# Optimization experiments

Measured on AMD Instinct MI355X. Metric: run time of the kernel, lower is better.

## Reference

```python
import jax, jax.numpy as jnp
import numpy as np

NU, NI, NR = 50000, 50000, 5   # users, items, rating levels
D, B, LS, LI = 64, 512, 32, 64 # embed_dim, batch, max social nbrs, max item hist
NEG = -1e9


def setup_inputs() -> dict:
    key = jax.random.key(0)
    ks = iter(jax.random.split(key, 64))
    def lin(din, dout):
        s = 1.0 / np.sqrt(din)
        return (jax.random.uniform(next(ks), (din, dout), minval=-s, maxval=s, dtype=jnp.float32),
                jax.random.uniform(next(ks), (dout,), minval=-s, maxval=s, dtype=jnp.float32))
    inp = {}
    inp['user_w'] = jax.random.normal(next(ks), (NU, D), dtype=jnp.float32) * 0.1
    inp['item_w'] = jax.random.normal(next(ks), (NI, D), dtype=jnp.float32) * 0.1
    inp['rating_w'] = jax.random.normal(next(ks), (NR, D), dtype=jnp.float32) * 0.1
    for name, din, dout in [('i_ln1', 2*D, D), ('i_ln2', D, D), ('i_ln3', 2*D, D),
                            ('i_att1', 2*D, D), ('i_att2', D, D), ('i_att3', D, 1),
                            ('s_ln1', D, D), ('s_ln2', 2*D, D), ('s_ln3', D, D),
                            ('s_att1', 2*D, D), ('s_att2', D, D), ('s_att3', D, 1)]:
        w, b = lin(din, dout)
        inp[name + '_w'] = w
        inp[name + '_b'] = b
    inp['nodes'] = jax.random.randint(next(ks), (B,), 0, NU)
    inp['social_hist'] = jax.random.randint(next(ks), (NU, LS), 0, NU)
    inp['social_mask'] = jax.random.bernoulli(next(ks), 0.5, (NU, LS)).at[:, 0].set(True)
    inp['item_hist'] = jax.random.randint(next(ks), (NU, LI), 0, NI)
    inp['rating_hist'] = jax.random.randint(next(ks), (NU, LI), 0, NR)
    inp['item_mask'] = jax.random.bernoulli(next(ks), 0.5, (NU, LI)).at[:, 0].set(True)
    return inp


def reference(user_w, item_w, rating_w,
              i_ln1_w, i_ln1_b, i_ln2_w, i_ln2_b, i_ln3_w, i_ln3_b,
              i_att1_w, i_att1_b, i_att2_w, i_att2_b, i_att3_w, i_att3_b,
              s_ln1_w, s_ln1_b, s_ln2_w, s_ln2_b, s_ln3_w, s_ln3_b,
              s_att1_w, s_att1_b, s_att2_w, s_att2_b, s_att3_w, s_att3_b,
              nodes, social_hist, social_mask, item_hist, rating_hist, item_mask):
    relu = jax.nn.relu

    def attn(x, w1, b1, w2, b2, w3, b3, mask):
        # x: [..., L, 2D] -> softmax weights over valid neighbors: [..., L]
        h = relu(x @ w1 + b1)
        h = relu(h @ w2 + b2)
        logit = (h @ w3 + b3)[..., 0]
        logit = jnp.where(mask, logit, NEG)
        return jax.nn.softmax(logit, axis=-1)

    def item_final(uids):
        # uids: any shape [...]; returns [..., D]  (Aggre_item.item_final)
        its, rts, m = item_hist[uids], rating_hist[uids], item_mask[uids]
        x = jnp.concatenate([item_w[its], rating_w[rts]], axis=-1)   # [...,LI,2D]
        x = relu(x @ i_ln1_w + i_ln1_b)                              # [...,LI,D]
        u = user_w[uids]                                             # [...,D]
        a_in = jnp.concatenate([x, jnp.broadcast_to(u[..., None, :], x.shape)], axis=-1)
        alpha = attn(a_in, i_att1_w, i_att1_b, i_att2_w, i_att2_b, i_att3_w, i_att3_b, m)
        hI = jnp.einsum('...l,...ld->...d', alpha, x)                # attention-weighted sum
        hI = relu(hI @ i_ln2_w + i_ln2_b)
        return relu(jnp.concatenate([u, hI], axis=-1) @ i_ln3_w + i_ln3_b)

    # item-space factor of query users
    hI_self = item_final(nodes)                                      # [B,D]
    # social aggregation: item_final over each user's social neighbors
    nbrs, nmask = social_hist[nodes], social_mask[nodes]             # [B,LS]
    hI_nb = item_final(nbrs)                                         # [B,LS,D]
    u = user_w[nodes]                                                # [B,D]
    b_in = jnp.concatenate([hI_nb, jnp.broadcast_to(u[:, None, :], hI_nb.shape)], axis=-1)
    beta = attn(b_in, s_att1_w, s_att1_b, s_att2_w, s_att2_b, s_att3_w, s_att3_b, nmask)
    hS = jnp.einsum('bl,bld->bd', beta, hI_nb)
    hS = relu(hS @ s_ln1_w + s_ln1_b)
    f = jnp.concatenate([hI_self, hS], axis=-1)
    f = relu(f @ s_ln2_w + s_ln2_b)
    return relu(f @ s_ln3_w + s_ln3_b)
```

## Files before the change

kernel.cpp:

```cpp
#include <hip/hip_runtime.h>
#include <math.h>


#define NII 50000
#define BB 512
#define LSS 32
#define NT 16896

typedef short short8 __attribute__((ext_vector_type(8)));
typedef float f32x4 __attribute__((ext_vector_type(4)));

static __device__ __forceinline__ bool mread(const void* p, long i, int mode) {
  if (mode == 0) return ((const int*)p)[i] != 0;
  if (mode == 2) return ((const float*)p)[i] != 0.0f;
  return ((const unsigned char*)p)[i] != 0;
}

static __device__ __forceinline__ float wsum(float v) {
#pragma unroll
  for (int s = 1; s < 64; s <<= 1) v += __shfl_xor(v, s);
  return v;
}
static __device__ __forceinline__ float wmax(float v) {
#pragma unroll
  for (int s = 1; s < 64; s <<= 1) v = fmaxf(v, __shfl_xor(v, s));
  return v;
}
static __device__ __forceinline__ float rsum16(float v) {
#pragma unroll
  for (int s = 1; s < 16; s <<= 1) v += __shfl_xor(v, s);
  return v;
}

static __device__ __forceinline__ short bf16rne(float f) {
  unsigned u = __float_as_uint(f);
  u = (u + 0x7FFFu + ((u >> 16) & 1u)) >> 16;
  return (short)u;
}
static __device__ __forceinline__ float bf16tof(short h) {
  return __uint_as_float(((unsigned)(unsigned short)h) << 16);
}

static __device__ __forceinline__ void wave_fence() {
  asm volatile("s_waitcnt lgkmcnt(0)" ::: "memory");
  __builtin_amdgcn_sched_barrier(0);
}

__global__ void setup_kernel(const unsigned int* __restrict__ sm,
                             int* __restrict__ flag,
                             const float* __restrict__ rating_w,
                             const float* __restrict__ w1,
                             const float* __restrict__ b1,
                             float* __restrict__ RW1g,
                             const float* __restrict__ A1w,
                             const float* __restrict__ A2w,
                             short* __restrict__ B1,
                             short* __restrict__ B2,
                             short* __restrict__ W1hi,
                             short* __restrict__ W1lo) {
  const int tid = threadIdx.x;
  if (blockIdx.x == 0) {
    __shared__ int notInt, notFloat;
    if (tid == 0) { notInt = 0; notFloat = 0; }
    __syncthreads();
    int ni = 0, nf = 0;
    for (int i = tid; i < 4096; i += 256) {
      unsigned int x = sm[i];
      if (x > 1u) ni = 1;
      if (x != 0u && x != 0x3F800000u) nf = 1;
    }
    if (ni) atomicOr(&notInt, 1);
    if (nf) atomicOr(&notFloat, 1);
    __syncthreads();
    if (tid == 0) flag[0] = notInt ? (notFloat ? 1 : 2) : 0;
  } else if (blockIdx.x == 1) {
    for (int t = tid; t < 320; t += 256) {
      const int r = t >> 6, c = t & 63;
      float acc = b1[c];
      for (int k = 0; k < 64; ++k)
        acc = fmaf(rating_w[r * 64 + k], w1[(64 + k) * 64 + c], acc);
      RW1g[r * 64 + c] = acc;
    }
  } else {
    for (int idx = tid; idx < 4096; idx += 256) {
      int e = idx & 7, g = idx >> 3;
      int l = g & 63, q = g >> 6;
      int kb = q >> 2, nb = q & 3;
      int k = kb * 32 + ((l >> 4) & 3) * 8 + e;
      int col = nb * 16 + (l & 15);
      B1[idx] = bf16rne(A1w[k * 64 + col]);
      B2[idx] = bf16rne(A2w[k * 64 + col]);
      float a = w1[k * 64 + col];
      short h = bf16rne(a);
      W1hi[idx] = h;
      W1lo[idx] = bf16rne(a - bf16tof(h));
    }
  }
}

__global__ void prepack2_kernel(const float* __restrict__ S1w,
                                const float* __restrict__ S2w,
                                short* __restrict__ B1,
                                short* __restrict__ B2) {
  for (int idx = threadIdx.x; idx < 4096; idx += 256) {
    int e = idx & 7, g = idx >> 3;
    int l = g & 63, q = g >> 6;
    int kb = q >> 2, nb = q & 3;
    int k = kb * 32 + ((l >> 4) & 3) * 8 + e;
    int col = nb * 16 + (l & 15);
    B1[idx] = bf16rne(S1w[k * 64 + col]);
    B2[idx] = bf16rne(S2w[k * 64 + col]);
  }
}

__global__ __launch_bounds__(256)
void pre_xbase_mfma_kernel(const float* __restrict__ item_w,
                           const short* __restrict__ W1hi,
                           const short* __restrict__ W1lo,
                           float* __restrict__ xbase) {
  const int lane = threadIdx.x & 63, w = threadIdx.x >> 6;
  const int l15 = lane & 15, lg4 = lane >> 4;
  short8 bh[8], bl[8];
#pragma unroll
  for (int q = 0; q < 8; ++q) {
    bh[q] = *(const short8*)(W1hi + (q * 64 + lane) * 8);
    bl[q] = *(const short8*)(W1lo + (q * 64 + lane) * 8);
  }
  const int wid = blockIdx.x * 4 + w;
  const int nw = gridDim.x * 4;
  for (int tile = wid; tile < 3125; tile += nw) {
    const long r0 = (long)tile * 16;
    const float* ap = item_w + (r0 + l15) * 64 + lg4 * 8;
    short8 ah[2], al[2];
#pragma unroll
    for (int kb = 0; kb < 2; ++kb) {
      const float4 a = *(const float4*)(ap + kb * 32);
      const float4 b = *(const float4*)(ap + kb * 32 + 4);
      float v[8] = {a.x, a.y, a.z, a.w, b.x, b.y, b.z, b.w};
      short8 hi, lo;
#pragma unroll
      for (int e = 0; e < 8; ++e) {
        short h = bf16rne(v[e]);
        hi[e] = h;
        lo[e] = bf16rne(v[e] - bf16tof(h));
      }
      ah[kb] = hi;
      al[kb] = lo;
    }
#pragma unroll
    for (int nb = 0; nb < 4; ++nb) {
      f32x4 acc = {0.0f, 0.0f, 0.0f, 0.0f};
      acc = __builtin_amdgcn_mfma_f32_16x16x32_bf16(ah[0], bh[0 * 4 + nb], acc, 0, 0, 0);
      acc = __builtin_amdgcn_mfma_f32_16x16x32_bf16(ah[1], bh[1 * 4 + nb], acc, 0, 0, 0);
      acc = __builtin_amdgcn_mfma_f32_16x16x32_bf16(ah[0], bl[0 * 4 + nb], acc, 0, 0, 0);
      acc = __builtin_amdgcn_mfma_f32_16x16x32_bf16(ah[1], bl[1 * 4 + nb], acc, 0, 0, 0);
      acc = __builtin_amdgcn_mfma_f32_16x16x32_bf16(al[0], bh[0 * 4 + nb], acc, 0, 0, 0);
      acc = __builtin_amdgcn_mfma_f32_16x16x32_bf16(al[1], bh[1 * 4 + nb], acc, 0, 0, 0);
#pragma unroll
      for (int r = 0; r < 4; ++r)
        xbase[(r0 + lg4 * 4 + r) * 64 + nb * 16 + l15] = acc[r];
    }
  }
}

__global__ void build_active_kernel(const int* __restrict__ nodes,
                                    const int* __restrict__ social_hist,
                                    const void* __restrict__ social_mask,
                                    const int* __restrict__ flagp,
                                    int* __restrict__ counter,
                                    int* __restrict__ list,
                                    int* __restrict__ aUid) {
  const int t = blockIdx.x * 256 + threadIdx.x;
  if (t >= NT) return;
  const int mode = flagp[0];
  int uid;
  bool active;
  if (t < BB) {
    active = true;
    uid = nodes[t];
  } else {
    int nb = t - BB;
    int b = nb >> 5, l = nb & 31;
    long mi = (long)nodes[b] * LSS + l;
    active = mread(social_mask, mi, mode);
    uid = active ? social_hist[mi] : 0;
  }
  if (active) {
    int pos = atomicAdd(counter, 1);
    list[pos] = t;
    aUid[pos] = uid;
  }
}

__global__ __launch_bounds__(256, 2)
void uA1_kernel(const float* __restrict__ user_w,
                const float* __restrict__ A1w, const float* __restrict__ A1b,
                const int* __restrict__ idxsrc, const int* __restrict__ nActp,
                float* __restrict__ uA1buf) {
  const int tid = threadIdx.x, lane = tid & 63, w = tid >> 6;
  const int i0 = blockIdx.x * 64;
  const int nA = nActp[0];
  if (i0 >= nA) return;
  __shared__ float sW[64][64], sU[64][64];
  __shared__ float sb[64];
  __shared__ int sUid[64];
  for (int i = tid; i < 4096; i += 256) sW[i >> 6][i & 63] = A1w[4096 + i];
  if (tid < 64) {
    sb[tid] = A1b[tid];
    sUid[tid] = (i0 + tid < nA) ? idxsrc[i0 + tid] : 0;
  }
  __syncthreads();
  for (int i = tid; i < 4096; i += 256) {
    int r = i >> 6, c = i & 63;
    sU[r][c] = user_w[(long)sUid[r] * 64 + c];
  }
  __syncthreads();
  float acc[16];
#pragma unroll
  for (int r = 0; r < 16; ++r) acc[r] = sb[lane];
  for (int k = 0; k < 64; k += 4) {
    float wv0 = sW[k][lane], wv1 = sW[k + 1][lane];
    float wv2 = sW[k + 2][lane], wv3 = sW[k + 3][lane];
#pragma unroll
    for (int r = 0; r < 16; ++r) {
      const float4 xv = *(const float4*)(&sU[w * 16 + r][k]);
      acc[r] = fmaf(xv.x, wv0, acc[r]);
      acc[r] = fmaf(xv.y, wv1, acc[r]);
      acc[r] = fmaf(xv.z, wv2, acc[r]);
      acc[r] = fmaf(xv.w, wv3, acc[r]);
    }
  }
#pragma unroll
  for (int r = 0; r < 16; ++r) {
    int row = i0 + w * 16 + r;
    if (row < nA) uA1buf[(long)row * 64 + lane] = acc[r];
  }
}

__global__ __launch_bounds__(512, 8)
void core_mfma_kernel(const float* __restrict__ xbase,
                      const float* __restrict__ RW1g,
                      const float* __restrict__ uA1buf,
                      const short* __restrict__ Bimg1,
                      const short* __restrict__ Bimg2,
                      const float* __restrict__ A2b,
                      const float* __restrict__ A3w,
                      const int* __restrict__ item_hist,
                      const int* __restrict__ rating_hist,
                      const void* __restrict__ item_mask,
                      const int* __restrict__ flagp,
                      const int* __restrict__ aUid,
                      const int* __restrict__ nActp,
                      float* __restrict__ hvecbuf) {
  __shared__ __align__(16) short sB1[4096], sB2[4096];
  __shared__ __align__(16) char smem[8][3072];
  const int tid = threadIdx.x, lane = tid & 63, w = tid >> 6;
  short* h1w = (short*)(smem[w]);
  float* lgw = (float*)(smem[w] + 2560);
  int* cw = (int*)(smem[w] + 2816);

  ((int4*)sB1)[tid] = ((const int4*)Bimg1)[tid];
  ((int4*)sB2)[tid] = ((const int4*)Bimg2)[tid];
  __syncthreads();

  const int mode = flagp[0];
  const int nA = nActp[0];
  const float a2bv = A2b[lane];
  const float a3v = A3w[lane];
  const int l15 = lane & 15;
  const int lg4 = lane >> 4;

#define B1F(q) (*(const short8*)(sB1 + ((q) * 64 + lane) * 8))
#define B2F(q) (*(const short8*)(sB2 + ((q) * 64 + lane) * 8))

  for (int idx = blockIdx.x * 8 + w; idx < nA; idx += gridDim.x * 8) {
    wave_fence();
    const long uid = aUid[idx];

    const long mbase = uid * 64;
    bool m = mread(item_mask, mbase + lane, mode);
    unsigned long long bal = __ballot(m);
    const int nact = (int)__popcll(bal);
    int pos = (int)__popcll(bal & ((1ull << lane) - 1ull));
    if (m) cw[pos] = (item_hist[mbase + lane] << 3) | rating_hist[mbase + lane];
    const float uA1v = uA1buf[(long)idx * 64 + lane];
    wave_fence();

    const int ng = (nact + 15) >> 4;
    for (int mc = 0; mc < ng; ++mc) {
      wave_fence();
      int row = mc * 16 + l15;
      if (row >= nact) row = nact - 1;
      const int p = cw[row];
      const long it = p >> 3;
      const int rt = p & 7;
      short8 xa[2];
#pragma unroll
      for (int kb = 0; kb < 2; ++kb) {
        const int koff = kb * 32 + lg4 * 8;
        const float* xp = xbase + it * 64 + koff;
        const float* rp = RW1g + rt * 64 + koff;
        const float4 a = *(const float4*)xp;
        const float4 b = *(const float4*)(xp + 4);
        const float4 c = *(const float4*)rp;
        const float4 d = *(const float4*)(rp + 4);
        short8 f;
        f[0] = bf16rne(fmaxf(a.x + c.x, 0.0f));
        f[1] = bf16rne(fmaxf(a.y + c.y, 0.0f));
        f[2] = bf16rne(fmaxf(a.z + c.z, 0.0f));
        f[3] = bf16rne(fmaxf(a.w + c.w, 0.0f));
        f[4] = bf16rne(fmaxf(b.x + d.x, 0.0f));
        f[5] = bf16rne(fmaxf(b.y + d.y, 0.0f));
        f[6] = bf16rne(fmaxf(b.z + d.z, 0.0f));
        f[7] = bf16rne(fmaxf(b.w + d.w, 0.0f));
        xa[kb] = f;
      }
#pragma unroll
      for (int nb = 0; nb < 4; ++nb) {
        const float ui = __shfl(uA1v, nb * 16 + l15);
        f32x4 acc = {ui, ui, ui, ui};
        acc = __builtin_amdgcn_mfma_f32_16x16x32_bf16(xa[0], B1F(0 * 4 + nb), acc, 0, 0, 0);
        acc = __builtin_amdgcn_mfma_f32_16x16x32_bf16(xa[1], B1F(1 * 4 + nb), acc, 0, 0, 0);
#pragma unroll
        for (int r = 0; r < 4; ++r)
          h1w[(lg4 * 4 + r) * 80 + nb * 16 + l15] = bf16rne(fmaxf(acc[r], 0.0f));
      }
      wave_fence();
      short8 ha[2];
      ha[0] = *(const short8*)(h1w + l15 * 80 + lg4 * 8);
      ha[1] = *(const short8*)(h1w + l15 * 80 + 32 + lg4 * 8);
      float t0 = 0.0f, t1 = 0.0f, t2 = 0.0f, t3 = 0.0f;
#pragma unroll
      for (int nb = 0; nb < 4; ++nb) {
        const float b2 = __shfl(a2bv, nb * 16 + l15);
        f32x4 acc = {b2, b2, b2, b2};
        acc = __builtin_amdgcn_mfma_f32_16x16x32_bf16(ha[0], B2F(0 * 4 + nb), acc, 0, 0, 0);
        acc = __builtin_amdgcn_mfma_f32_16x16x32_bf16(ha[1], B2F(1 * 4 + nb), acc, 0, 0, 0);
        const float a3c = __shfl(a3v, nb * 16 + l15);
        t0 = fmaf(fmaxf(acc[0], 0.0f), a3c, t0);
        t1 = fmaf(fmaxf(acc[1], 0.0f), a3c, t1);
        t2 = fmaf(fmaxf(acc[2], 0.0f), a3c, t2);
        t3 = fmaf(fmaxf(acc[3], 0.0f), a3c, t3);
      }
      t0 = rsum16(t0); t1 = rsum16(t1); t2 = rsum16(t2); t3 = rsum16(t3);
      if (l15 == 0) {
        const int jb = mc * 16 + lg4 * 4;
        lgw[jb + 0] = t0;
        lgw[jb + 1] = t1;
        lgw[jb + 2] = t2;
        lgw[jb + 3] = t3;
      }
    }
    wave_fence();

    const bool valid = (lane < nact);
    float lv = valid ? lgw[lane] : -1e30f;
    float mx = wmax(lv);
    float e = valid ? __expf(lv - mx) : 0.0f;
    float s = wsum(e);
    const float alpha = e / s;

    float hi = 0.0f;
    for (int j = 0; j < nact; ++j) {
      const float aj = __shfl(alpha, j);
      const int p = cw[j];
      const float xv =
          fmaxf(xbase[(long)(p >> 3) * 64 + lane] + RW1g[(p & 7) * 64 + lane], 0.0f);
      hi = fmaf(aj, xv, hi);
    }
    hvecbuf[(long)idx * 64 + lane] = hi;
  }
#undef B1F
#undef B2F
}

__global__ __launch_bounds__(256, 2)
void hI2final_kernel(const float* __restrict__ hvecbuf,
                     const float* __restrict__ user_w,
                     const float* __restrict__ W2w, const float* __restrict__ W2b,
                     const float* __restrict__ W3w, const float* __restrict__ W3b,
                     const int* __restrict__ list, const int* __restrict__ aUid,
                     const int* __restrict__ nActp, float* __restrict__ hIbuf) {
  const int tid = threadIdx.x, lane = tid & 63, w = tid >> 6;
  const int i0 = blockIdx.x * 32;
  const int nA = nActp[0];
  if (i0 >= nA) return;
  __shared__ float sW[128][64];
  __shared__ float sX[32][128];
  __shared__ float sb[64];
  __shared__ int sUid[32], sInst[32];
  for (int i = tid; i < 4096; i += 256) sW[i >> 6][i & 63] = W2w[i];
  if (tid < 64) sb[tid] = W2b[tid];
  if (tid < 32) {
    bool ok = (i0 + tid) < nA;
    sUid[tid] = ok ? aUid[i0 + tid] : 0;
    sInst[tid] = ok ? list[i0 + tid] : 0;
  }
  __syncthreads();
  for (int i = tid; i < 2048; i += 256) {
    int r = i >> 6, c = i & 63;
    sX[r][64 + c] = (i0 + r < nA) ? hvecbuf[(long)(i0 + r) * 64 + c] : 0.0f;
    sX[r][c] = user_w[(long)sUid[r] * 64 + c];
  }
  __syncthreads();

  float acc[8];
  {
    const float bv = sb[lane];
#pragma unroll
    for (int r = 0; r < 8; ++r) acc[r] = bv;
    for (int k = 0; k < 64; k += 4) {
      float wv0 = sW[k][lane], wv1 = sW[k + 1][lane];
      float wv2 = sW[k + 2][lane], wv3 = sW[k + 3][lane];
#pragma unroll
      for (int r = 0; r < 8; ++r) {
        const float4 xv = *(const float4*)(&sX[w * 8 + r][64 + k]);
        acc[r] = fmaf(xv.x, wv0, acc[r]);
        acc[r] = fmaf(xv.y, wv1, acc[r]);
        acc[r] = fmaf(xv.z, wv2, acc[r]);
        acc[r] = fmaf(xv.w, wv3, acc[r]);
      }
    }
#pragma unroll
    for (int r = 0; r < 8; ++r) sX[w * 8 + r][64 + lane] = fmaxf(acc[r], 0.0f);
  }
  __syncthreads();
  for (int i = tid; i < 8192; i += 256) sW[i >> 6][i & 63] = W3w[i];
  if (tid < 64) sb[tid] = W3b[tid];
  __syncthreads();

  {
    const float bv = sb[lane];
#pragma unroll
    for (int r = 0; r < 8; ++r) acc[r] = bv;
    for (int k = 0; k < 128; k += 4) {
      float wv0 = sW[k][lane], wv1 = sW[k + 1][lane];
      float wv2 = sW[k + 2][lane], wv3 = sW[k + 3][lane];
#pragma unroll
      for (int r = 0; r < 8; ++r) {
        const float4 xv = *(const float4*)(&sX[w * 8 + r][k]);
        acc[r] = fmaf(xv.x, wv0, acc[r]);
        acc[r] = fmaf(xv.y, wv1, acc[r]);
        acc[r] = fmaf(xv.z, wv2, acc[r]);
        acc[r] = fmaf(xv.w, wv3, acc[r]);
      }
    }
#pragma unroll
    for (int r = 0; r < 8; ++r) {
      int row = i0 + w * 8 + r;
      if (row < nA)
        hIbuf[(long)sInst[w * 8 + r] * 64 + lane] = fmaxf(acc[r], 0.0f);
    }
  }
}

__global__ __launch_bounds__(256, 8)
void social_fused_kernel(const float* __restrict__ hIbuf,
                         const float* __restrict__ user_w,
                         const float* __restrict__ S1w,
                         const float* __restrict__ S1b,
                         const short* __restrict__ S1img,
                         const short* __restrict__ S2img,
                         const float* __restrict__ S2b,
                         const float* __restrict__ S3w,
                         const float* __restrict__ L1w, const float* __restrict__ L1b,
                         const float* __restrict__ L2w, const float* __restrict__ L2b,
                         const float* __restrict__ L3w, const float* __restrict__ L3b,
                         const int* __restrict__ nodes,
                         const void* __restrict__ social_mask,
                         const int* __restrict__ flagp,
                         float* __restrict__ out) {
  __shared__ __align__(16) short sB1[4096], sB2[4096];
  __shared__ __align__(16) char smem[4][3584];
  const int tid = threadIdx.x, lane = tid & 63, w = tid >> 6;
  short* h1w = (short*)(smem[w]);
  float* lgw = (float*)(smem[w] + 2560);
  int* cw = (int*)(smem[w] + 2816);
  float* vA = (float*)(smem[w] + 3072);
  float* vB = (float*)(smem[w] + 3328);

  for (int i = tid; i < 512; i += 256) {
    ((int4*)sB1)[i] = ((const int4*)S1img)[i];
    ((int4*)sB2)[i] = ((const int4*)S2img)[i];
  }
  __syncthreads();

  const int mode = flagp[0];
  const int l15 = lane & 15;
  const int lg4 = lane >> 4;
  const int b = blockIdx.x * 4 + w;
  const long uid = nodes[b];

  bool m = (lane < LSS) ? mread(social_mask, uid * LSS + lane, mode) : false;
  unsigned long long bal = __ballot(m);
  const int nval = (int)__popcll(bal);
  int pos = (int)__popcll(bal & ((1ull << lane) - 1ull));
  if (m) cw[pos] = lane;

  const float uv = user_w[uid * 64 + lane];
  float uA1v = S1b[lane];
#pragma unroll 8
  for (int k = 0; k < 64; ++k)
    uA1v = fmaf(__shfl(uv, k), S1w[(64 + k) * 64 + lane], uA1v);
  const float a2bv = S2b[lane];
  const float a3v = S3w[lane];
  wave_fence();

  const long hbase = 512L + (long)b * 32;
  const int ng = (nval + 15) >> 4;
  for (int mc = 0; mc < ng; ++mc) {
    wave_fence();
    int row = mc * 16 + l15;
    if (row >= nval) row = nval - 1;
    const long hrow = hbase + cw[row];
    short8 xa[2];
#pragma unroll
    for (int kb = 0; kb < 2; ++kb) {
      const float* xp = hIbuf + hrow * 64 + kb * 32 + lg4 * 8;
      const float4 a = *(const float4*)xp;
      const float4 bb = *(const float4*)(xp + 4);
      short8 f;
      f[0] = bf16rne(a.x);  f[1] = bf16rne(a.y);
      f[2] = bf16rne(a.z);  f[3] = bf16rne(a.w);
      f[4] = bf16rne(bb.x); f[5] = bf16rne(bb.y);
      f[6] = bf16rne(bb.z); f[7] = bf16rne(bb.w);
      xa[kb] = f;
    }
#pragma unroll
    for (int nb = 0; nb < 4; ++nb) {
      const float ui = __shfl(uA1v, nb * 16 + l15);
      f32x4 acc = {ui, ui, ui, ui};
      acc = __builtin_amdgcn_mfma_f32_16x16x32_bf16(
          xa[0], *(const short8*)(sB1 + ((0 * 4 + nb) * 64 + lane) * 8), acc, 0, 0, 0);
      acc = __builtin_amdgcn_mfma_f32_16x16x32_bf16(
          xa[1], *(const short8*)(sB1 + ((1 * 4 + nb) * 64 + lane) * 8), acc, 0, 0, 0);
#pragma unroll
      for (int r = 0; r < 4; ++r)
        h1w[(lg4 * 4 + r) * 80 + nb * 16 + l15] = bf16rne(fmaxf(acc[r], 0.0f));
    }
    wave_fence();
    short8 ha[2];
    ha[0] = *(const short8*)(h1w + l15 * 80 + lg4 * 8);
    ha[1] = *(const short8*)(h1w + l15 * 80 + 32 + lg4 * 8);
    float t0 = 0.0f, t1 = 0.0f, t2 = 0.0f, t3 = 0.0f;
#pragma unroll
    for (int nb = 0; nb < 4; ++nb) {
      const float b2 = __shfl(a2bv, nb * 16 + l15);
      f32x4 acc = {b2, b2, b2, b2};
      acc = __builtin_amdgcn_mfma_f32_16x16x32_bf16(
          ha[0], *(const short8*)(sB2 + ((0 * 4 + nb) * 64 + lane) * 8), acc, 0, 0, 0);
      acc = __builtin_amdgcn_mfma_f32_16x16x32_bf16(
          ha[1], *(const short8*)(sB2 + ((1 * 4 + nb) * 64 + lane) * 8), acc, 0, 0, 0);
      const float a3c = __shfl(a3v, nb * 16 + l15);
      t0 = fmaf(fmaxf(acc[0], 0.0f), a3c, t0);
      t1 = fmaf(fmaxf(acc[1], 0.0f), a3c, t1);
      t2 = fmaf(fmaxf(acc[2], 0.0f), a3c, t2);
      t3 = fmaf(fmaxf(acc[3], 0.0f), a3c, t3);
    }
    t0 = rsum16(t0); t1 = rsum16(t1); t2 = rsum16(t2); t3 = rsum16(t3);
    if (l15 == 0) {
      const int jb = mc * 16 + lg4 * 4;
      lgw[jb + 0] = t0;
      lgw[jb + 1] = t1;
      lgw[jb + 2] = t2;
      lgw[jb + 3] = t3;
    }
  }
  wave_fence();

  const bool valid = (lane < nval);
  float lv = valid ? lgw[lane] : -1e30f;
  float mx = wmax(lv);
  float e = valid ? __expf(lv - mx) : 0.0f;
  float s = wsum(e);
  const float beta = e / s;

  float hs = 0.0f;
  for (int j = 0; j < nval; ++j) {
    const float bj = __shfl(beta, j);
    hs = fmaf(bj, hIbuf[(hbase + cw[j]) * 64 + lane], hs);
  }

  vA[lane] = hs;
  wave_fence();
  float acc = L1b[lane];
#pragma unroll 8
  for (int k = 0; k < 64; ++k) acc = fmaf(vA[k], L1w[k * 64 + lane], acc);
  const float vecB = fmaxf(acc, 0.0f);
  const float selfv = hIbuf[(long)b * 64 + lane];
  wave_fence();
  vA[lane] = selfv;
  vB[lane] = vecB;
  wave_fence();
  acc = L2b[lane];
#pragma unroll 8
  for (int k = 0; k < 64; ++k) acc = fmaf(vA[k], L2w[k * 64 + lane], acc);
#pragma unroll 8
  for (int k = 0; k < 64; ++k) acc = fmaf(vB[k], L2w[(64 + k) * 64 + lane], acc);
  const float fv = fmaxf(acc, 0.0f);
  wave_fence();
  vA[lane] = fv;
  wave_fence();
  acc = L3b[lane];
#pragma unroll 8
  for (int k = 0; k < 64; ++k) acc = fmaf(vA[k], L3w[k * 64 + lane], acc);
  out[(long)b * 64 + lane] = fmaxf(acc, 0.0f);
}

extern "C" void kernel_launch(void* const* d_in, const int* in_sizes, int n_in,
                              void* d_out, int out_size, void* d_ws, size_t ws_size,
                              hipStream_t stream) {
  const float* user_w   = (const float*)d_in[0];
  const float* item_w   = (const float*)d_in[1];
  const float* rating_w = (const float*)d_in[2];
  const float* i_ln1_w  = (const float*)d_in[3];
  const float* i_ln1_b  = (const float*)d_in[4];
  const float* i_ln2_w  = (const float*)d_in[5];
  const float* i_ln2_b  = (const float*)d_in[6];
  const float* i_ln3_w  = (const float*)d_in[7];
  const float* i_ln3_b  = (const float*)d_in[8];
  const float* i_att1_w = (const float*)d_in[9];
  const float* i_att1_b = (const float*)d_in[10];
  const float* i_att2_w = (const float*)d_in[11];
  const float* i_att2_b = (const float*)d_in[12];
  const float* i_att3_w = (const float*)d_in[13];
  const float* i_att3_b = (const float*)d_in[14];
  const float* s_ln1_w  = (const float*)d_in[15];
  const float* s_ln1_b  = (const float*)d_in[16];
  const float* s_ln2_w  = (const float*)d_in[17];
  const float* s_ln2_b  = (const float*)d_in[18];
  const float* s_ln3_w  = (const float*)d_in[19];
  const float* s_ln3_b  = (const float*)d_in[20];
  const float* s_att1_w = (const float*)d_in[21];
  const float* s_att1_b = (const float*)d_in[22];
  const float* s_att2_w = (const float*)d_in[23];
  const float* s_att2_b = (const float*)d_in[24];
  const float* s_att3_w = (const float*)d_in[25];
  const float* s_att3_b = (const float*)d_in[26];
  const int*  nodes       = (const int*)d_in[27];
  const int*  social_hist = (const int*)d_in[28];
  const void* social_mask = d_in[29];
  const int*  item_hist   = (const int*)d_in[30];
  const int*  rating_hist = (const int*)d_in[31];
  const void* item_mask   = d_in[32];

  char* ws = (char*)d_ws;
  int*   flag    = (int*)(ws + 0);
  int*   counter = (int*)(ws + 256);
  int*   list    = (int*)(ws + 512);
  int*   aUid    = (int*)(ws + 68096);
  float* uA1buf  = (float*)(ws + 135680);
  float* hvecbuf = (float*)(ws + 4461056);
  float* hIbuf   = hvecbuf;
  short* W1hi    = (short*)(ws + 4461056);
  short* W1lo    = (short*)(ws + 4469248);
  float* xbase   = (float*)(ws + 8786432);
  short* S1img   = (short*)(ws + 8786432);
  short* S2img   = (short*)(ws + 8794624);
  float* RW1g    = (float*)(ws + 21586432);
  short* Bimg1   = (short*)(ws + 21587712);
  short* Bimg2   = (short*)(ws + 21595904);

  hipMemsetAsync(counter, 0, 4, stream);
  setup_kernel<<<3, 256, 0, stream>>>((const unsigned int*)social_mask, flag,
                                      rating_w, i_ln1_w, i_ln1_b, RW1g,
                                      i_att1_w, i_att2_w, Bimg1, Bimg2, W1hi, W1lo);
  pre_xbase_mfma_kernel<<<512, 256, 0, stream>>>(item_w, W1hi, W1lo, xbase);
  build_active_kernel<<<NT / 256, 256, 0, stream>>>(
      nodes, social_hist, social_mask, flag, counter, list, aUid);
  uA1_kernel<<<NT / 64, 256, 0, stream>>>(user_w, i_att1_w, i_att1_b,
                                          aUid, counter, uA1buf);
  core_mfma_kernel<<<NT / 16, 512, 0, stream>>>(
      xbase, RW1g, uA1buf, Bimg1, Bimg2, i_att2_b, i_att3_w,
      item_hist, rating_hist, item_mask, flag, aUid, counter, hvecbuf);
  prepack2_kernel<<<1, 256, 0, stream>>>(s_att1_w, s_att2_w, S1img, S2img);
  hI2final_kernel<<<NT / 32, 256, 0, stream>>>(
      hvecbuf, user_w, i_ln2_w, i_ln2_b, i_ln3_w, i_ln3_b,
      list, aUid, counter, hIbuf);
  social_fused_kernel<<<BB / 4, 256, 0, stream>>>(
      hIbuf, user_w, s_att1_w, s_att1_b, S1img, S2img, s_att2_b, s_att3_w,
      s_ln1_w, s_ln1_b, s_ln2_w, s_ln2_b, s_ln3_w, s_ln3_b,
      nodes, social_mask, flag, (float*)d_out);
}
```

Before: 130.0 us.

## Fuse online softmax and weighted aggregation into MFMA chunk loop

Replaces the post-loop softmax and second gather pass over item/rating embeddings with an online-softmax accumulation done per 16-row chunk. The ReLU'd inputs already loaded for the MFMA are kept in fp32 registers and accumulated with running max and sum rescaling, then reduced across the 16-lane groups at the end. This removes a second round of scattered global reads per active user. In exchange it adds register pressure (16-element accumulator plus 16-element input copy), more shuffles per chunk, and lowers the occupancy hint in launch bounds from 8 to 6.

New measurement: 127.9 us. Within noise of the previous version (-1.6%).

```diff
diff --git a/kernel.cpp b/kernel.cpp
--- a/kernel.cpp
+++ b/kernel.cpp
@@ -29,6 +29,11 @@
 static __device__ __forceinline__ float rsum16(float v) {
 #pragma unroll
   for (int s = 1; s < 16; s <<= 1) v += __shfl_xor(v, s);
+  return v;
+}
+static __device__ __forceinline__ float rmax16(float v) {
+#pragma unroll
+  for (int s = 1; s < 16; s <<= 1) v = fmaxf(v, __shfl_xor(v, s));
   return v;
 }
 
@@ -237,7 +242,7 @@
   }
 }
 
-__global__ __launch_bounds__(512, 8)
+__global__ __launch_bounds__(512, 6)
 void core_mfma_kernel(const float* __restrict__ xbase,
                       const float* __restrict__ RW1g,
                       const float* __restrict__ uA1buf,
@@ -258,6 +263,7 @@
   short* h1w = (short*)(smem[w]);
   float* lgw = (float*)(smem[w] + 2560);
   int* cw = (int*)(smem[w] + 2816);
+  float* vAw = (float*)(smem[w]);
 
   ((int4*)sB1)[tid] = ((const int4*)Bimg1)[tid];
   ((int4*)sB2)[tid] = ((const int4*)Bimg2)[tid];
@@ -278,23 +284,29 @@
     const long uid = aUid[idx];
 
     const long mbase = uid * 64;
-    bool m = mread(item_mask, mbase + lane, mode);
-    unsigned long long bal = __ballot(m);
+    bool mk = mread(item_mask, mbase + lane, mode);
+    unsigned long long bal = __ballot(mk);
     const int nact = (int)__popcll(bal);
     int pos = (int)__popcll(bal & ((1ull << lane) - 1ull));
-    if (m) cw[pos] = (item_hist[mbase + lane] << 3) | rating_hist[mbase + lane];
+    if (mk) cw[pos] = (item_hist[mbase + lane] << 3) | rating_hist[mbase + lane];
     const float uA1v = uA1buf[(long)idx * 64 + lane];
     wave_fence();
+
+    float m = -1e30f, s = 0.0f;
+    float hIa[16];
+#pragma unroll
+    for (int q = 0; q < 16; ++q) hIa[q] = 0.0f;
 
     const int ng = (nact + 15) >> 4;
     for (int mc = 0; mc < ng; ++mc) {
       wave_fence();
       int row = mc * 16 + l15;
+      const bool valid = (row < nact);
       if (row >= nact) row = nact - 1;
       const int p = cw[row];
       const long it = p >> 3;
       const int rt = p & 7;
-      short8 xa[2];
+      float xf[16];
 #pragma unroll
       for (int kb = 0; kb < 2; ++kb) {
         const int koff = kb * 32 + lg4 * 8;
@@ -304,15 +316,21 @@
         const float4 b = *(const float4*)(xp + 4);
         const float4 c = *(const float4*)rp;
         const float4 d = *(const float4*)(rp + 4);
+        xf[kb * 8 + 0] = fmaxf(a.x + c.x, 0.0f);
+        xf[kb * 8 + 1] = fmaxf(a.y + c.y, 0.0f);
+        xf[kb * 8 + 2] = fmaxf(a.z + c.z, 0.0f);
+        xf[kb * 8 + 3] = fmaxf(a.w + c.w, 0.0f);
+        xf[kb * 8 + 4] = fmaxf(b.x + d.x, 0.0f);
+        xf[kb * 8 + 5] = fmaxf(b.y + d.y, 0.0f);
+        xf[kb * 8 + 6] = fmaxf(b.z + d.z, 0.0f);
+        xf[kb * 8 + 7] = fmaxf(b.w + d.w, 0.0f);
+      }
+      short8 xa[2];
+#pragma unroll
+      for (int kb = 0; kb < 2; ++kb) {
         short8 f;
-        f[0] = bf16rne(fmaxf(a.x + c.x, 0.0f));
-        f[1] = bf16rne(fmaxf(a.y + c.y, 0.0f));
-        f[2] = bf16rne(fmaxf(a.z + c.z, 0.0f));
-        f[3] = bf16rne(fmaxf(a.w + c.w, 0.0f));
-        f[4] = bf16rne(fmaxf(b.x + d.x, 0.0f));
-        f[5] = bf16rne(fmaxf(b.y + d.y, 0.0f));
-        f[6] = bf16rne(fmaxf(b.z + d.z, 0.0f));
-        f[7] = bf16rne(fmaxf(b.w + d.w, 0.0f));
+#pragma unroll
+        for (int e = 0; e < 8; ++e) f[e] = bf16rne(xf[kb * 8 + e]);
         xa[kb] = f;
       }
 #pragma unroll
@@ -344,31 +362,38 @@
       }
       t0 = rsum16(t0); t1 = rsum16(t1); t2 = rsum16(t2); t3 = rsum16(t3);
       if (l15 == 0) {
-        const int jb = mc * 16 + lg4 * 4;
+        const int jb = lg4 * 4;
         lgw[jb + 0] = t0;
         lgw[jb + 1] = t1;
         lgw[jb + 2] = t2;
         lgw[jb + 3] = t3;
       }
+      wave_fence();
+      const float lv = valid ? lgw[l15] : -1e30f;
+      const float cm = rmax16(lv);
+      const float mn = fmaxf(m, cm);
+      const float scale = __expf(m - mn);
+      const float e = valid ? __expf(lv - mn) : 0.0f;
+      const float cs = rsum16(e);
+      s = s * scale + cs;
+      m = mn;
+#pragma unroll
+      for (int q = 0; q < 16; ++q) hIa[q] = fmaf(hIa[q], scale, e * xf[q]);
     }
     wave_fence();
 
-    const bool valid = (lane < nact);
-    float lv = valid ? lgw[lane] : -1e30f;
-    float mx = wmax(lv);
-    float e = valid ? __expf(lv - mx) : 0.0f;
-    float s = wsum(e);
-    const float alpha = e / s;
-
-    float hi = 0.0f;
-    for (int j = 0; j < nact; ++j) {
-      const float aj = __shfl(alpha, j);
-      const int p = cw[j];
-      const float xv =
-          fmaxf(xbase[(long)(p >> 3) * 64 + lane] + RW1g[(p & 7) * 64 + lane], 0.0f);
-      hi = fmaf(aj, xv, hi);
-    }
-    hvecbuf[(long)idx * 64 + lane] = hi;
+    const float inv = 1.0f / s;
+#pragma unroll
+    for (int q = 0; q < 16; ++q) hIa[q] = rsum16(hIa[q] * inv);
+    if (l15 == 0) {
+#pragma unroll
+      for (int e = 0; e < 8; ++e) {
+        vAw[lg4 * 8 + e] = hIa[e];
+        vAw[32 + lg4 * 8 + e] = hIa[8 + e];
+      }
+    }
+    wave_fence();
+    hvecbuf[(long)idx * 64 + lane] = vAw[lane];
   }
 #undef B1F
 #undef B2F
```

## Fold active-list build into setup, drop prepack kernel, restructure core and final kernels

Applied to the files above, without the earlier changes.

Merges build_active into setup_kernel, with each extra block recomputing the mask-type flag locally. Removes prepack2_kernel by packing the social attention weights to bf16 inside social_fused_kernel. Changes core_mfma_kernel from a grid-stride loop to one wave per active item, with early exit for empty blocks and a 4-way unrolled weighted gather. hI2final now keeps both weight matrices in shared memory and loops over 4 row groups per block. The aim is fewer launches and less repeated weight staging, at the cost of redundant flag scans and more shared memory per block.

Result: slower. 141.5 us (+8.8%).

```diff
diff --git a/kernel.cpp b/kernel.cpp
--- a/kernel.cpp
+++ b/kernel.cpp
@@ -57,7 +57,12 @@
                              short* __restrict__ B1,
                              short* __restrict__ B2,
                              short* __restrict__ W1hi,
-                             short* __restrict__ W1lo) {
+                             short* __restrict__ W1lo,
+                             const int* __restrict__ nodes,
+                             const int* __restrict__ social_hist,
+                             int* __restrict__ counter,
+                             int* __restrict__ list,
+                             int* __restrict__ aUid) {
   const int tid = threadIdx.x;
   if (blockIdx.x == 0) {
     __shared__ int notInt, notFloat;
@@ -81,7 +86,7 @@
         acc = fmaf(rating_w[r * 64 + k], w1[(64 + k) * 64 + c], acc);
       RW1g[r * 64 + c] = acc;
     }
-  } else {
+  } else if (blockIdx.x == 2) {
     for (int idx = tid; idx < 4096; idx += 256) {
       int e = idx & 7, g = idx >> 3;
       int l = g & 63, q = g >> 6;
@@ -95,21 +100,40 @@
       W1hi[idx] = h;
       W1lo[idx] = bf16rne(a - bf16tof(h));
     }
-  }
-}
-
-__global__ void prepack2_kernel(const float* __restrict__ S1w,
-                                const float* __restrict__ S2w,
-                                short* __restrict__ B1,
-                                short* __restrict__ B2) {
-  for (int idx = threadIdx.x; idx < 4096; idx += 256) {
-    int e = idx & 7, g = idx >> 3;
-    int l = g & 63, q = g >> 6;
-    int kb = q >> 2, nb = q & 3;
-    int k = kb * 32 + ((l >> 4) & 3) * 8 + e;
-    int col = nb * 16 + (l & 15);
-    B1[idx] = bf16rne(S1w[k * 64 + col]);
-    B2[idx] = bf16rne(S2w[k * 64 + col]);
+  } else {
+    __shared__ int nI, nF;
+    if (tid == 0) { nI = 0; nF = 0; }
+    __syncthreads();
+    int ni = 0, nf = 0;
+    for (int i = tid; i < 4096; i += 256) {
+      unsigned int x = sm[i];
+      if (x > 1u) ni = 1;
+      if (x != 0u && x != 0x3F800000u) nf = 1;
+    }
+    if (ni) atomicOr(&nI, 1);
+    if (nf) atomicOr(&nF, 1);
+    __syncthreads();
+    const int mode = nI ? (nF ? 1 : 2) : 0;
+    const int t = (blockIdx.x - 3) * 256 + tid;
+    if (t < NT) {
+      int uid;
+      bool active;
+      if (t < BB) {
+        active = true;
+        uid = nodes[t];
+      } else {
+        int nb = t - BB;
+        int b = nb >> 5, l = nb & 31;
+        long mi = (long)nodes[b] * LSS + l;
+        active = mread((const void*)sm, mi, mode);
+        uid = active ? social_hist[mi] : 0;
+      }
+      if (active) {
+        int pos = atomicAdd(counter, 1);
+        list[pos] = t;
+        aUid[pos] = uid;
+      }
+    }
   }
 }
 
@@ -160,35 +184,6 @@
       for (int r = 0; r < 4; ++r)
         xbase[(r0 + lg4 * 4 + r) * 64 + nb * 16 + l15] = acc[r];
     }
-  }
-}
-
-__global__ void build_active_kernel(const int* __restrict__ nodes,
-                                    const int* __restrict__ social_hist,
-                                    const void* __restrict__ social_mask,
-                                    const int* __restrict__ flagp,
-                                    int* __restrict__ counter,
-                                    int* __restrict__ list,
-                                    int* __restrict__ aUid) {
-  const int t = blockIdx.x * 256 + threadIdx.x;
-  if (t >= NT) return;
-  const int mode = flagp[0];
-  int uid;
-  bool active;
-  if (t < BB) {
-    active = true;
-    uid = nodes[t];
-  } else {
-    int nb = t - BB;
-    int b = nb >> 5, l = nb & 31;
-    long mi = (long)nodes[b] * LSS + l;
-    active = mread(social_mask, mi, mode);
-    uid = active ? social_hist[mi] : 0;
-  }
-  if (active) {
-    int pos = atomicAdd(counter, 1);
-    list[pos] = t;
-    aUid[pos] = uid;
   }
 }
 
@@ -255,6 +250,9 @@
   __shared__ __align__(16) short sB1[4096], sB2[4096];
   __shared__ __align__(16) char smem[8][3072];
   const int tid = threadIdx.x, lane = tid & 63, w = tid >> 6;
+  const int nA = nActp[0];
+  if (blockIdx.x * 8 >= nA) return;
+
   short* h1w = (short*)(smem[w]);
   float* lgw = (float*)(smem[w] + 2560);
   int* cw = (int*)(smem[w] + 2816);
@@ -263,8 +261,10 @@
   ((int4*)sB2)[tid] = ((const int4*)Bimg2)[tid];
   __syncthreads();
 
+  const int idx = blockIdx.x * 8 + w;
+  if (idx >= nA) return;
+
   const int mode = flagp[0];
-  const int nA = nActp[0];
   const float a2bv = A2b[lane];
   const float a3v = A3w[lane];
   const int l15 = lane & 15;
@@ -273,103 +273,113 @@
 #define B1F(q) (*(const short8*)(sB1 + ((q) * 64 + lane) * 8))
 #define B2F(q) (*(const short8*)(sB2 + ((q) * 64 + lane) * 8))
 
-  for (int idx = blockIdx.x * 8 + w; idx < nA; idx += gridDim.x * 8) {
+  const long uid = aUid[idx];
+
+  const long mbase = uid * 64;
+  bool mk = mread(item_mask, mbase + lane, mode);
+  unsigned long long bal = __ballot(mk);
+  const int nact = (int)__popcll(bal);
+  int pos = (int)__popcll(bal & ((1ull << lane) - 1ull));
+  if (mk) cw[pos] = (item_hist[mbase + lane] << 3) | rating_hist[mbase + lane];
+  const float uA1v = uA1buf[(long)idx * 64 + lane];
+  wave_fence();
+
+  const int ng = (nact + 15) >> 4;
+  for (int mc = 0; mc < ng; ++mc) {
     wave_fence();
-    const long uid = aUid[idx];
-
-    const long mbase = uid * 64;
-    bool m = mread(item_mask, mbase + lane, mode);
-    unsigned long long bal = __ballot(m);
-    const int nact = (int)__popcll(bal);
-    int pos = (int)__popcll(bal & ((1ull << lane) - 1ull));
-    if (m) cw[pos] = (item_hist[mbase + lane] << 3) | rating_hist[mbase + lane];
-    const float uA1v = uA1buf[(long)idx * 64 + lane];
+    int row = mc * 16 + l15;
+    if (row >= nact) row = nact - 1;
+    const int p = cw[row];
+    const long it = p >> 3;
+    const int rt = p & 7;
+    short8 xa[2];
+#pragma unroll
+    for (int kb = 0; kb < 2; ++kb) {
+      const int koff = kb * 32 + lg4 * 8;
+      const float* xp = xbase + it * 64 + koff;
+      const float* rp = RW1g + rt * 64 + koff;
+      const float4 a = *(const float4*)xp;
+      const float4 b = *(const float4*)(xp + 4);
+      const float4 c = *(const float4*)rp;
+      const float4 d = *(const float4*)(rp + 4);
+      short8 f;
+      f[0] = bf16rne(fmaxf(a.x + c.x, 0.0f));
+      f[1] = bf16rne(fmaxf(a.y + c.y, 0.0f));
+      f[2] = bf16rne(fmaxf(a.z + c.z, 0.0f));
+      f[3] = bf16rne(fmaxf(a.w + c.w, 0.0f));
+      f[4] = bf16rne(fmaxf(b.x + d.x, 0.0f));
+      f[5] = bf16rne(fmaxf(b.y + d.y, 0.0f));
+      f[6] = bf16rne(fmaxf(b.z + d.z, 0.0f));
+      f[7] = bf16rne(fmaxf(b.w + d.w, 0.0f));
+      xa[kb] = f;
+    }
+#pragma unroll
+    for (int nb = 0; nb < 4; ++nb) {
+      const float ui = __shfl(uA1v, nb * 16 + l15);
+      f32x4 acc = {ui, ui, ui, ui};
+      acc = __builtin_amdgcn_mfma_f32_16x16x32_bf16(xa[0], B1F(0 * 4 + nb), acc, 0, 0, 0);
+      acc = __builtin_amdgcn_mfma_f32_16x16x32_bf16(xa[1], B1F(1 * 4 + nb), acc, 0, 0, 0);
+#pragma unroll
+      for (int r = 0; r < 4; ++r)
+        h1w[(lg4 * 4 + r) * 80 + nb * 16 + l15] = bf16rne(fmaxf(acc[r], 0.0f));
+    }
     wave_fence();
-
-    const int ng = (nact + 15) >> 4;
-    for (int mc = 0; mc < ng; ++mc) {
-      wave_fence();
-      int row = mc * 16 + l15;
-      if (row >= nact) row = nact - 1;
-      const int p = cw[row];
-      const long it = p >> 3;
-      const int rt = p & 7;
-      short8 xa[2];
-#pragma unroll
-      for (int kb = 0; kb < 2; ++kb) {
-        const int koff = kb * 32 + lg4 * 8;
-        const float* xp = xbase + it * 64 + koff;
-        const float* rp = RW1g + rt * 64 + koff;
-        const float4 a = *(const float4*)xp;
-        const float4 b = *(const float4*)(xp + 4);
-        const float4 c = *(const float4*)rp;
-        const float4 d = *(const float4*)(rp + 4);
-        short8 f;
-        f[0] = bf16rne(fmaxf(a.x + c.x, 0.0f));
-        f[1] = bf16rne(fmaxf(a.y + c.y, 0.0f));
-        f[2] = bf16rne(fmaxf(a.z + c.z, 0.0f));
-        f[3] = bf16rne(fmaxf(a.w + c.w, 0.0f));
-        f[4] = bf16rne(fmaxf(b.x + d.x, 0.0f));
-        f[5] = bf16rne(fmaxf(b.y + d.y, 0.0f));
-        f[6] = bf16rne(fmaxf(b.z + d.z, 0.0f));
-        f[7] = bf16rne(fmaxf(b.w + d.w, 0.0f));
-        xa[kb] = f;
-      }
-#pragma unroll
-      for (int nb = 0; nb < 4; ++nb) {
-        const float ui = __shfl(uA1v, nb * 16 + l15);
-        f32x4 acc = {ui, ui, ui, ui};
-        acc = __builtin_amdgcn_mfma_f32_16x16x32_bf16(xa[0], B1F(0 * 4 + nb), acc, 0, 0, 0);
-        acc = __builtin_amdgcn_mfma_f32_16x16x32_bf16(xa[1], B1F(1 * 4 + nb), acc, 0, 0, 0);
-#pragma unroll
-        for (int r = 0; r < 4; ++r)
-          h1w[(lg4 * 4 + r) * 80 + nb * 16 + l15] = bf16rne(fmaxf(acc[r], 0.0f));
-      }
-      wave_fence();
-      short8 ha[2];
-      ha[0] = *(const short8*)(h1w + l15 * 80 + lg4 * 8);
-      ha[1] = *(const short8*)(h1w + l15 * 80 + 32 + lg4 * 8);
-      float t0 = 0.0f, t1 = 0.0f, t2 = 0.0f, t3 = 0.0f;
-#pragma unroll
-      for (int nb = 0; nb < 4; ++nb) {
-        const float b2 = __shfl(a2bv, nb * 16 + l15);
-        f32x4 acc = {b2, b2, b2, b2};
-        acc = __builtin_amdgcn_mfma_f32_16x16x32_bf16(ha[0], B2F(0 * 4 + nb), acc, 0, 0, 0);
-        acc = __builtin_amdgcn_mfma_f32_16x16x32_bf16(ha[1], B2F(1 * 4 + nb), acc, 0, 0, 0);
-        const float a3c = __shfl(a3v, nb * 16 + l15);
-        t0 = fmaf(fmaxf(acc[0], 0.0f), a3c, t0);
-        t1 = fmaf(fmaxf(acc[1], 0.0f), a3c, t1);
-        t2 = fmaf(fmaxf(acc[2], 0.0f), a3c, t2);
-        t3 = fmaf(fmaxf(acc[3], 0.0f), a3c, t3);
-      }
-      t0 = rsum16(t0); t1 = rsum16(t1); t2 = rsum16(t2); t3 = rsum16(t3);
-      if (l15 == 0) {
-        const int jb = mc * 16 + lg4 * 4;
-        lgw[jb + 0] = t0;
-        lgw[jb + 1] = t1;
-        lgw[jb + 2] = t2;
-        lgw[jb + 3] = t3;
-      }
-    }
-    wave_fence();
-
-    const bool valid = (lane < nact);
-    float lv = valid ? lgw[lane] : -1e30f;
-    float mx = wmax(lv);
-    float e = valid ? __expf(lv - mx) : 0.0f;
-    float s = wsum(e);
-    const float alpha = e / s;
-
-    float hi = 0.0f;
-    for (int j = 0; j < nact; ++j) {
-      const float aj = __shfl(alpha, j);
-      const int p = cw[j];
-      const float xv =
-          fmaxf(xbase[(long)(p >> 3) * 64 + lane] + RW1g[(p & 7) * 64 + lane], 0.0f);
-      hi = fmaf(aj, xv, hi);
-    }
-    hvecbuf[(long)idx * 64 + lane] = hi;
-  }
+    short8 ha[2];
+    ha[0] = *(const short8*)(h1w + l15 * 80 + lg4 * 8);
+    ha[1] = *(const short8*)(h1w + l15 * 80 + 32 + lg4 * 8);
+    float t0 = 0.0f, t1 = 0.0f, t2 = 0.0f, t3 = 0.0f;
+#pragma unroll
+    for (int nb = 0; nb < 4; ++nb) {
+      const float b2 = __shfl(a2bv, nb * 16 + l15);
+      f32x4 acc = {b2, b2, b2, b2};
+      acc = __builtin_amdgcn_mfma_f32_16x16x32_bf16(ha[0], B2F(0 * 4 + nb), acc, 0, 0, 0);
+      acc = __builtin_amdgcn_mfma_f32_16x16x32_bf16(ha[1], B2F(1 * 4 + nb), acc, 0, 0, 0);
+      const float a3c = __shfl(a3v, nb * 16 + l15);
+      t0 = fmaf(fmaxf(acc[0], 0.0f), a3c, t0);
+      t1 = fmaf(fmaxf(acc[1], 0.0f), a3c, t1);
+      t2 = fmaf(fmaxf(acc[2], 0.0f), a3c, t2);
+      t3 = fmaf(fmaxf(acc[3], 0.0f), a3c, t3);
+    }
+    t0 = rsum16(t0); t1 = rsum16(t1); t2 = rsum16(t2); t3 = rsum16(t3);
+    if (l15 == 0) {
+      const int jb = mc * 16 + lg4 * 4;
+      lgw[jb + 0] = t0;
+      lgw[jb + 1] = t1;
+      lgw[jb + 2] = t2;
+      lgw[jb + 3] = t3;
+    }
+  }
+  wave_fence();
+
+  const bool valid = (lane < nact);
+  float lv = valid ? lgw[lane] : -1e30f;
+  float mx = wmax(lv);
+  float e = valid ? __expf(lv - mx) : 0.0f;
+  float s = wsum(e);
+  const float alpha = e / s;
+
+  float h0 = 0.0f, hA = 0.0f, hB = 0.0f, hC = 0.0f;
+  int j = 0;
+  for (; j + 3 < nact; j += 4) {
+    const int p0 = cw[j], p1 = cw[j + 1], p2 = cw[j + 2], p3 = cw[j + 3];
+    const float a0 = __shfl(alpha, j), a1 = __shfl(alpha, j + 1);
+    const float a2 = __shfl(alpha, j + 2), a3 = __shfl(alpha, j + 3);
+    const float x0 = xbase[(long)(p0 >> 3) * 64 + lane] + RW1g[(p0 & 7) * 64 + lane];
+    const float x1 = xbase[(long)(p1 >> 3) * 64 + lane] + RW1g[(p1 & 7) * 64 + lane];
+    const float x2 = xbase[(long)(p2 >> 3) * 64 + lane] + RW1g[(p2 & 7) * 64 + lane];
+    const float x3 = xbase[(long)(p3 >> 3) * 64 + lane] + RW1g[(p3 & 7) * 64 + lane];
+    h0 = fmaf(a0, fmaxf(x0, 0.0f), h0);
+    hA = fmaf(a1, fmaxf(x1, 0.0f), hA);
+    hB = fmaf(a2, fmaxf(x2, 0.0f), hB);
+    hC = fmaf(a3, fmaxf(x3, 0.0f), hC);
+  }
+  for (; j < nact; ++j) {
+    const int p = cw[j];
+    const float aj = __shfl(alpha, j);
+    const float xv = xbase[(long)(p >> 3) * 64 + lane] + RW1g[(p & 7) * 64 + lane];
+    h0 = fmaf(aj, fmaxf(xv, 0.0f), h0);
+  }
+  hvecbuf[(long)idx * 64 + lane] = (h0 + hA) + (hB + hC);
 #undef B1F
 #undef B2F
 }
@@ -382,74 +392,76 @@
                      const int* __restrict__ list, const int* __restrict__ aUid,
                      const int* __restrict__ nActp, float* __restrict__ hIbuf) {
   const int tid = threadIdx.x, lane = tid & 63, w = tid >> 6;
-  const int i0 = blockIdx.x * 32;
   const int nA = nActp[0];
-  if (i0 >= nA) return;
-  __shared__ float sW[128][64];
+  if (blockIdx.x * 128 >= nA) return;
+  __shared__ float sW2[64][64];
+  __shared__ float sW3[128][64];
   __shared__ float sX[32][128];
-  __shared__ float sb[64];
+  __shared__ float sb2[64], sb3[64];
   __shared__ int sUid[32], sInst[32];
-  for (int i = tid; i < 4096; i += 256) sW[i >> 6][i & 63] = W2w[i];
-  if (tid < 64) sb[tid] = W2b[tid];
-  if (tid < 32) {
-    bool ok = (i0 + tid) < nA;
-    sUid[tid] = ok ? aUid[i0 + tid] : 0;
-    sInst[tid] = ok ? list[i0 + tid] : 0;
-  }
-  __syncthreads();
-  for (int i = tid; i < 2048; i += 256) {
-    int r = i >> 6, c = i & 63;
-    sX[r][64 + c] = (i0 + r < nA) ? hvecbuf[(long)(i0 + r) * 64 + c] : 0.0f;
-    sX[r][c] = user_w[(long)sUid[r] * 64 + c];
-  }
-  __syncthreads();
-
-  float acc[8];
-  {
-    const float bv = sb[lane];
-#pragma unroll
-    for (int r = 0; r < 8; ++r) acc[r] = bv;
-    for (int k = 0; k < 64; k += 4) {
-      float wv0 = sW[k][lane], wv1 = sW[k + 1][lane];
-      float wv2 = sW[k + 2][lane], wv3 = sW[k + 3][lane];
+  for (int i = tid; i < 4096; i += 256) sW2[i >> 6][i & 63] = W2w[i];
+  for (int i = tid; i < 8192; i += 256) sW3[i >> 6][i & 63] = W3w[i];
+  if (tid < 64) { sb2[tid] = W2b[tid]; sb3[tid] = W3b[tid]; }
+
+  for (int g2 = 0; g2 < 4; ++g2) {
+    const int i0 = (blockIdx.x * 4 + g2) * 32;
+    if (i0 >= nA) break;
+    __syncthreads();
+    if (tid < 32) {
+      bool ok = (i0 + tid) < nA;
+      sUid[tid] = ok ? aUid[i0 + tid] : 0;
+      sInst[tid] = ok ? list[i0 + tid] : 0;
+    }
+    __syncthreads();
+    for (int i = tid; i < 2048; i += 256) {
+      int r = i >> 6, c = i & 63;
+      sX[r][64 + c] = (i0 + r < nA) ? hvecbuf[(long)(i0 + r) * 64 + c] : 0.0f;
+      sX[r][c] = user_w[(long)sUid[r] * 64 + c];
+    }
+    __syncthreads();
+
+    float acc[8];
+    {
+      const float bv = sb2[lane];
+#pragma unroll
+      for (int r = 0; r < 8; ++r) acc[r] = bv;
+      for (int k = 0; k < 64; k += 4) {
+        float wv0 = sW2[k][lane], wv1 = sW2[k + 1][lane];
+        float wv2 = sW2[k + 2][lane], wv3 = sW2[k + 3][lane];
+#pragma unroll
+        for (int r = 0; r < 8; ++r) {
+          const float4 xv = *(const float4*)(&sX[w * 8 + r][64 + k]);
+          acc[r] = fmaf(xv.x, wv0, acc[r]);
+          acc[r] = fmaf(xv.y, wv1, acc[r]);
+          acc[r] = fmaf(xv.z, wv2, acc[r]);
+          acc[r] = fmaf(xv.w, wv3, acc[r]);
+        }
+      }
+#pragma unroll
+      for (int r = 0; r < 8; ++r) sX[w * 8 + r][64 + lane] = fmaxf(acc[r], 0.0f);
+    }
+    {
+      const float bv = sb3[lane];
+#pragma unroll
+      for (int r = 0; r < 8; ++r) acc[r] = bv;
+      for (int k = 0; k < 128; k += 4) {
+        float wv0 = sW3[k][lane], wv1 = sW3[k + 1][lane];
+        float wv2 = sW3[k + 2][lane], wv3 = sW3[k + 3][lane];
+#pragma unroll
+        for (int r = 0; r < 8; ++r) {
+          const float4 xv = *(const float4*)(&sX[w * 8 + r][k]);
+          acc[r] = fmaf(xv.x, wv0, acc[r]);
+          acc[r] = fmaf(xv.y, wv1, acc[r]);
+          acc[r] = fmaf(xv.z, wv2, acc[r]);
+          acc[r] = fmaf(xv.w, wv3, acc[r]);
+        }
+      }
 #pragma unroll
       for (int r = 0; r < 8; ++r) {
-        const float4 xv = *(const float4*)(&sX[w * 8 + r][64 + k]);
-        acc[r] = fmaf(xv.x, wv0, acc[r]);
-        acc[r] = fmaf(xv.y, wv1, acc[r]);
-        acc[r] = fmaf(xv.z, wv2, acc[r]);
-        acc[r] = fmaf(xv.w, wv3, acc[r]);
+        int row = i0 + w * 8 + r;
+        if (row < nA)
+          hIbuf[(long)sInst[w * 8 + r] * 64 + lane] = fmaxf(acc[r], 0.0f);
       }
-    }
-#pragma unroll
-    for (int r = 0; r < 8; ++r) sX[w * 8 + r][64 + lane] = fmaxf(acc[r], 0.0f);
-  }
-  __syncthreads();
-  for (int i = tid; i < 8192; i += 256) sW[i >> 6][i & 63] = W3w[i];
-  if (tid < 64) sb[tid] = W3b[tid];
-  __syncthreads();
-
-  {
-    const float bv = sb[lane];
-#pragma unroll
-    for (int r = 0; r < 8; ++r) acc[r] = bv;
-    for (int k = 0; k < 128; k += 4) {
-      float wv0 = sW[k][lane], wv1 = sW[k + 1][lane];
-      float wv2 = sW[k + 2][lane], wv3 = sW[k + 3][lane];
-#pragma unroll
-      for (int r = 0; r < 8; ++r) {
-        const float4 xv = *(const float4*)(&sX[w * 8 + r][k]);
-        acc[r] = fmaf(xv.x, wv0, acc[r]);
-        acc[r] = fmaf(xv.y, wv1, acc[r]);
-        acc[r] = fmaf(xv.z, wv2, acc[r]);
-        acc[r] = fmaf(xv.w, wv3, acc[r]);
-      }
-    }
-#pragma unroll
-    for (int r = 0; r < 8; ++r) {
-      int row = i0 + w * 8 + r;
-      if (row < nA)
-        hIbuf[(long)sInst[w * 8 + r] * 64 + lane] = fmaxf(acc[r], 0.0f);
     }
   }
 }
@@ -459,8 +471,7 @@
                          const float* __restrict__ user_w,
                          const float* __restrict__ S1w,
                          const float* __restrict__ S1b,
-                         const short* __restrict__ S1img,
-                         const short* __restrict__ S2img,
+                         const float* __restrict__ S2w,
                          const float* __restrict__ S2b,
                          const float* __restrict__ S3w,
                          const float* __restrict__ L1w, const float* __restrict__ L1b,
@@ -479,9 +490,14 @@
   float* vA = (float*)(smem[w] + 3072);
   float* vB = (float*)(smem[w] + 3328);
 
-  for (int i = tid; i < 512; i += 256) {
-    ((int4*)sB1)[i] = ((const int4*)S1img)[i];
-    ((int4*)sB2)[i] = ((const int4*)S2img)[i];
+  for (int i = tid; i < 4096; i += 256) {
+    int e = i & 7, g = i >> 3;
+    int l = g & 63, q = g >> 6;
+    int kb = q >> 2, nb = q & 3;
+    int k = kb * 32 + ((l >> 4) & 3) * 8 + e;
+    int col = nb * 16 + (l & 15);
+    sB1[i] = bf16rne(S1w[k * 64 + col]);
+    sB2[i] = bf16rne(S2w[k * 64 + col]);
   }
   __syncthreads();
 
@@ -655,30 +671,27 @@
   short* W1hi    = (short*)(ws + 4461056);
   short* W1lo    = (short*)(ws + 4469248);
   float* xbase   = (float*)(ws + 8786432);
-  short* S1img   = (short*)(ws + 8786432);
-  short* S2img   = (short*)(ws + 8794624);
   float* RW1g    = (float*)(ws + 21586432);
   short* Bimg1   = (short*)(ws + 21587712);
   short* Bimg2   = (short*)(ws + 21595904);
 
   hipMemsetAsync(counter, 0, 4, stream);
-  setup_kernel<<<3, 256, 0, stream>>>((const unsigned int*)social_mask, flag,
-                                      rating_w, i_ln1_w, i_ln1_b, RW1g,
-                                      i_att1_w, i_att2_w, Bimg1, Bimg2, W1hi, W1lo);
+  setup_kernel<<<3 + NT / 256, 256, 0, stream>>>(
+      (const unsigned int*)social_mask, flag,
+      rating_w, i_ln1_w, i_ln1_b, RW1g,
+      i_att1_w, i_att2_w, Bimg1, Bimg2, W1hi, W1lo,
+      nodes, social_hist, counter, list, aUid);
   pre_xbase_mfma_kernel<<<512, 256, 0, stream>>>(item_w, W1hi, W1lo, xbase);
-  build_active_kernel<<<NT / 256, 256, 0, stream>>>(
-      nodes, social_hist, social_mask, flag, counter, list, aUid);
   uA1_kernel<<<NT / 64, 256, 0, stream>>>(user_w, i_att1_w, i_att1_b,
                                           aUid, counter, uA1buf);
-  core_mfma_kernel<<<NT / 16, 512, 0, stream>>>(
+  core_mfma_kernel<<<NT / 8, 512, 0, stream>>>(
       xbase, RW1g, uA1buf, Bimg1, Bimg2, i_att2_b, i_att3_w,
       item_hist, rating_hist, item_mask, flag, aUid, counter, hvecbuf);
-  prepack2_kernel<<<1, 256, 0, stream>>>(s_att1_w, s_att2_w, S1img, S2img);
-  hI2final_kernel<<<NT / 32, 256, 0, stream>>>(
+  hI2final_kernel<<<NT / 128, 256, 0, stream>>>(
       hvecbuf, user_w, i_ln2_w, i_ln2_b, i_ln3_w, i_ln3_b,
       list, aUid, counter, hIbuf);
   social_fused_kernel<<<BB / 4, 256, 0, stream>>>(
-      hIbuf, user_w, s_att1_w, s_att1_b, S1img, S2img, s_att2_b, s_att3_w,
+      hIbuf, user_w, s_att1_w, s_att1_b, s_att2_w, s_att2_b, s_att3_w,
       s_ln1_w, s_ln1_b, s_ln2_w, s_ln2_b, s_ln3_w, s_ln3_b,
       nodes, social_mask, flag, (float*)d_out);
 }
```
